# Kernel tuning notes

Hardware: AMD Instinct MI355X
Metric: run time of the kernel (lower is better)

The kernel has to match this reference:

```python
import jax, jax.numpy as jnp
import numpy as np
from jax import lax

RATE = 2
KSIZE = 3
FUSE_K = 3
SOFTMAX_SCALE = 10.0
EPS = 1e-8


def extract_patches(x, k, s):
    """ZeroPad2d(1) then unfold: x [B,C,H,W] -> patches [B, oh*ow, C, k, k]."""
    xp = jnp.pad(x, ((0, 0), (0, 0), (1, 1), (1, 1)))
    B, C, Hp, Wp = xp.shape
    oh = (Hp - k) // s + 1
    ow = (Wp - k) // s + 1
    ii = (jnp.arange(oh) * s)[:, None] + jnp.arange(k)[None, :]   # [oh,k]
    jj = (jnp.arange(ow) * s)[:, None] + jnp.arange(k)[None, :]   # [ow,k]
    p = xp[:, :, ii[:, :, None, None], jj[None, None, :, :]]      # [B,C,oh,k,ow,k]
    p = p.transpose(0, 2, 4, 1, 3, 5).reshape(B, oh * ow, C, k, k)
    return p


def _fuse_conv(a, eye):
    # a: [B,1,N,M]; 3x3 identity-diagonal smoothing conv, padding 1
    return lax.conv_general_dilated(a, eye, (1, 1), [(1, 1), (1, 1)],
                                    dimension_numbers=('NCHW', 'OIHW', 'NCHW'))


def contextual_attention(in_data, mask):
    B, C, H, W = in_data.shape
    Cf = C // 2
    f_full = in_data[:, :Cf]          # narrow(1,0,C//2)
    b_full = in_data[:, :Cf]          # source narrows the SAME slice for b
    mask_f = mask.astype(in_data.dtype)
    rate = RATE
    kernel = 2 * rate

    # raw 4x4 patches of full-res background (deconv filters), [B,L,Cf,4,4]
    raw_w = extract_patches(b_full, kernel, rate)

    # nearest downsample by 1/rate == strided slicing
    f = f_full[:, :, ::rate, ::rate]
    b = b_full[:, :, ::rate, ::rate]
    h, w = f.shape[2], f.shape[3]
    L = h * w

    # 3x3 matching patches of downsampled background, L2-normalized per patch
    wpat = extract_patches(b, KSIZE, 1)                              # [B,L,Cf,3,3]
    norm = jnp.sqrt(jnp.sum(wpat * wpat, axis=(2, 3, 4), keepdims=True))
    wn = wpat / jnp.maximum(norm, EPS)

    # per-sample conv2d(xi, wi_normed, padding=1) == patch/patch correlation
    fp = extract_patches(f, KSIZE, 1)                                # [B,hw,Cf,3,3]
    yi = jnp.einsum('bpckl,bqckl->bqp', fp, wn).reshape(B, L, h, w)  # [B,L,h,w]

    # fuse: two diagonal 3x3 smoothing passes over the [L, h*w] score matrix
    eye = jnp.eye(FUSE_K, dtype=in_data.dtype).reshape(1, 1, FUSE_K, FUSE_K)
    A = yi.reshape(B, 1, L, h * w)
    A = _fuse_conv(A, eye)
    A = A.reshape(B, h, w, h, w).transpose(0, 2, 1, 4, 3).reshape(B, 1, w * h, w * h)
    A = _fuse_conv(A, eye)
    A = A.reshape(B, w, h, w, h).transpose(0, 2, 1, 4, 3)
    yi = A.reshape(B, L, h, w)

    # mask gate: mm = 1 where the 3x3 mask patch is all-zero
    mpat = extract_patches(mask_f, KSIZE, 1)[0]                      # [L,1,3,3]
    m_mean = jnp.mean(mpat, axis=(1, 2, 3))                          # [L]
    mm = (m_mean == 0.0).astype(in_data.dtype)[None, :, None, None]
    yi = yi * mm
    yi = jax.nn.softmax(yi * SOFTMAX_SCALE, axis=1)
    yi = yi * mm

    # conv_transpose2d(yi, raw_wi, stride=rate, padding=1) / 4 per sample
    def agg(y1, rw):
        rhs = jnp.flip(rw, (-2, -1)).transpose(1, 0, 2, 3)           # [Cf,L,4,4]
        return lax.conv_general_dilated(y1[None], rhs, (1, 1), [(2, 2), (2, 2)],
                                        lhs_dilation=(rate, rate),
                                        dimension_numbers=('NCHW', 'OIHW', 'NCHW'))[0]
    y = jax.vmap(agg)(yi, raw_w) / 4.0                               # [B,Cf,H,W]

    # masked_fill_(inv_mask, 0) == multiply by {0,1} mask, upsampled to H x W
    mask_up = jnp.repeat(jnp.repeat(mask_f, rate, axis=2), rate, axis=3)
    y = y * mask_up

    return jnp.concatenate([b_full, f_full, y], axis=1)             # [B,3*Cf,H,W]


def setup_inputs() -> dict:
    key = jax.random.key(0)
    k1, k2 = jax.random.split(key)
    in_data = jax.random.normal(k1, (2, 128, 128, 128), dtype=jnp.float32)
    mask = jax.random.randint(k2, (1, 1, 64, 64), 0, 2, dtype=jnp.int32)
    return {"in_data": in_data, "mask": mask}


def reference(in_data, mask):
    return contextual_attention(in_data, mask)
```

## Files before the change

kernel.cpp:

```cpp
#include <hip/hip_runtime.h>
#include <math.h>

#define MAX_SLOTS 64
#define L 4096

#define OFF_CNT   0
#define OFF_LIST  64
#define OFF_FSUB  512
#define OFF_K5    2230784
#define OFF_SF    4065792

__global__ __launch_bounds__(256) void k_init(const float* __restrict__ in,
                                              const int* __restrict__ mask,
                                              int* __restrict__ cnt,
                                              int* __restrict__ list,
                                              float* __restrict__ fsub,
                                              float* __restrict__ sf) {
    int idx = blockIdx.x * 256 + threadIdx.x;
    int j = idx & 63;
    int i = (idx >> 6) & 63;
    int c = (idx >> 12) & 63;
    int b = idx >> 18;
    float v = in[(((b * 128 + c) * 128) + 2 * i) * 128 + 2 * j];
    fsub[(size_t)b * 278784 + c * 4356 + (i + 1) * 66 + (j + 1)] = v;
    sf[idx] = 0.f;
    if (idx < 33280) {
        int plane = idx / 260;
        int r = idx - plane * 260;
        int pb = plane >> 6, pc = plane & 63;
        int row, col;
        if (r < 66) { row = 0; col = r; }
        else if (r < 132) { row = 65; col = r - 66; }
        else { int rr = r - 132; row = (rr >> 1) + 1; col = (rr & 1) ? 65 : 0; }
        fsub[(size_t)pb * 278784 + pc * 4356 + row * 66 + col] = 0.f;
    }
    if (blockIdx.x == 0) {
        __shared__ int lcnt;
        if (threadIdx.x == 0) lcnt = 0;
        __syncthreads();
        for (int q = threadIdx.x; q < L; q += 256) {
            int qi = q >> 6, qj = q & 63;
            bool allz = true;
            for (int dy = -1; dy <= 1; ++dy)
                for (int dx = -1; dx <= 1; ++dx) {
                    int y = qi + dy, x = qj + dx;
                    if (y >= 0 && y < 64 && x >= 0 && x < 64)
                        allz = allz && (mask[y * 64 + x] == 0);
                }
            if (allz) {
                int p = atomicAdd(&lcnt, 1);
                if (p < MAX_SLOTS) list[p] = q;
            }
        }
        __syncthreads();
        if (threadIdx.x == 0) *cnt = (lcnt < MAX_SLOTS) ? lcnt : MAX_SLOTS;
    }
}

__global__ __launch_bounds__(256) void k_mid(const int* __restrict__ cnt,
                                             const int* __restrict__ list,
                                             const float* __restrict__ fsub,
                                             float* __restrict__ K5,
                                             float* __restrict__ sf) {
    __shared__ float smem[5184];
    __shared__ int iflags[16];
    int tid = threadIdx.x;
    int blk = blockIdx.x;
    int nact = min(*cnt, MAX_SLOTS);

    if (blk < 128) {
        int slot = blk & 63, b = blk >> 6;
        if (slot >= nact) {
            for (int t = tid; t < 1600; t += 256) {
                int c = t / 25, e = t - c * 25;
                K5[(((size_t)b * 64 + c) * 64 + slot) * 28 + e] = 0.f;
            }
            return;
        }
        float* patch9 = smem;
        if (tid < 9) iflags[tid] = 0;
        __syncthreads();
        int Q = list[slot];
        const float* F = fsub + (size_t)b * 278784;
        int w = tid >> 6, lane = tid & 63;
        for (int combo = w; combo < 9; combo += 4) {
            int d2 = combo / 3 - 1, d1 = combo % 3 - 1;
            int XQ = ((Q & 63) << 6) + (Q >> 6) + d2;
            if (XQ < 0 || XQ >= L) continue;
            int YQ = ((XQ & 63) << 6) + (XQ >> 6);
            int R = YQ + d1;
            if (R < 0 || R >= L) continue;
            if (lane == 0) iflags[combo] = 1;
            int ri = R >> 6, rj = R & 63;
            const float* Fp = F + ri * 66 + rj;
            float vals[9]; float ss = 0.f;
            #pragma unroll
            for (int k = 0; k < 9; ++k) {
                int t = lane + (k << 6);
                int c = t / 9; int tap = t - c * 9;
                int dy = tap / 3, dx = tap - dy * 3;
                float v = Fp[c * 4356 + dy * 66 + dx];
                vals[k] = v; ss += v * v;
            }
            for (int o = 32; o > 0; o >>= 1) ss += __shfl_xor(ss, o);
            float inv = 1.f / fmaxf(sqrtf(ss), 1e-8f);
            float* dst = patch9 + combo * 576;
            #pragma unroll
            for (int k = 0; k < 9; ++k) dst[lane + (k << 6)] = vals[k] * inv;
        }
        __syncthreads();
        for (int t = tid; t < 1600; t += 256) {
            int c = t / 25, e = t - c * 25;
            int oy = e / 5 - 2, ox = e - (e / 5) * 5 - 2;
            float s = 0.f;
            for (int dy = -1; dy <= 1; ++dy) {
                int dd2 = oy - dy; if (dd2 < -1 || dd2 > 1) continue;
                for (int dx = -1; dx <= 1; ++dx) {
                    int dd1 = ox - dx; if (dd1 < -1 || dd1 > 1) continue;
                    int combo = (dd2 + 1) * 3 + (dd1 + 1);
                    if (iflags[combo])
                        s += patch9[combo * 576 + c * 9 + (dy + 1) * 3 + (dx + 1)];
                }
            }
            K5[(((size_t)b * 64 + c) * 64 + slot) * 28 + e] = s;
        }
        return;
    }

    int bt = blk - 128;
    int combo = bt % 9; int rest = bt / 9;
    int slot = rest & 63, b = rest >> 6;
    if (slot >= nact) return;
    int d2 = combo / 3 - 1, d1 = combo % 3 - 1;
    int Q = list[slot];
    int XQ = ((Q & 63) << 6) + (Q >> 6) + d2;
    if (XQ < 0 || XQ >= L) return;
    int YQ = ((XQ & 63) << 6) + (XQ >> 6);
    int R = YQ + d1;
    if (R < 0 || R >= L) return;
    int ri = R >> 6, rj = R & 63;
    const float* F = fsub + (size_t)b * 278784;
    float* patch = smem;
    float* red = smem + 576;
    const float* Fp = F + ri * 66 + rj;
    auto ld = [&](int t) -> float {
        int c = t / 9; int tap = t - c * 9;
        int dy = tap / 3, dx = tap - dy * 3;
        return Fp[c * 4356 + dy * 66 + dx];
    };
    float v0 = ld(tid), v1 = ld(tid + 256), v2 = (tid < 64) ? ld(tid + 512) : 0.f;
    red[tid] = v0 * v0 + v1 * v1 + v2 * v2;
    __syncthreads();
    if (tid < 64) {
        float a = red[tid] + red[tid + 64] + red[tid + 128] + red[tid + 192];
        for (int o = 32; o > 0; o >>= 1) a += __shfl_xor(a, o);
        if (tid == 0) smem[832] = 1.f / fmaxf(sqrtf(a), 1e-8f);
    }
    __syncthreads();
    float inv = smem[832];
    patch[tid] = v0 * inv; patch[tid + 256] = v1 * inv;
    if (tid < 64) patch[tid + 512] = v2 * inv;
    __syncthreads();
    if (tid >= 252) return;
    int i, j;
    if (tid < 64)       { i = 0;  j = tid; }
    else if (tid < 128) { i = 63; j = tid - 64; }
    else if (tid < 190) { i = tid - 127; j = 0; }
    else                { i = tid - 189; j = 63; }
    int P = (i << 6) + j;
    int XP = (j << 6) + i + d2;
    if (XP < 0 || XP >= L) return;
    int YP = ((XP & 63) << 6) + (XP >> 6);
    int Z = YP + d1;
    if (Z < 0 || Z >= L) return;
    int pi = Z >> 6, pj = Z & 63;
    const float* Fz = F + pi * 66 + pj;
    float dot = 0.f;
    #pragma unroll 4
    for (int c = 0; c < 64; ++c) {
        const float* Fc = Fz + c * 4356;
        const float* pc = patch + c * 9;
        dot += Fc[0] * pc[0]   + Fc[1] * pc[1]   + Fc[2] * pc[2];
        dot += Fc[66] * pc[3]  + Fc[67] * pc[4]  + Fc[68] * pc[5];
        dot += Fc[132] * pc[6] + Fc[133] * pc[7] + Fc[134] * pc[8];
    }
    atomicAdd(&sf[((size_t)b * 64 + slot) * 4096 + P], dot);
}

__global__ __launch_bounds__(256) void k_conv(const float* __restrict__ fsub,
                                              const int* __restrict__ cnt,
                                              const float* __restrict__ K5,
                                              float* __restrict__ sf) {
    int nact = min(*cnt, MAX_SLOTS);
    if (nact == 0) return;
    int wid = __builtin_amdgcn_readfirstlane(blockIdx.x * 4 + (threadIdx.x >> 6));
    int j = threadIdx.x & 63;
    int r   = 1 + (wid % 62);
    int cg2 = (wid / 62) & 15;
    int b   = wid / 992;
    int jc = min(max(j, 1), 62);
    const float* F = fsub + (size_t)b * 278784;
    int base = (r - 1) * 66 + (jc - 1);
    bool active = (j >= 1 && j <= 62);
    int P = (r << 6) + j;
    for (int s0 = 0; s0 < nact; s0 += 16) {
        float acc[16];
        #pragma unroll
        for (int s = 0; s < 16; ++s) acc[s] = 0.f;
        #pragma unroll
        for (int cc = 0; cc < 4; ++cc) {
            int c = cg2 * 4 + cc;
            const float* Fc = F + c * 4356 + base;
            float win[25];
            #pragma unroll
            for (int dy = 0; dy < 5; ++dy)
                #pragma unroll
                for (int dx = 0; dx < 5; ++dx)
                    win[dy * 5 + dx] = Fc[dy * 66 + dx];
            const float* kc = K5 + (((size_t)b * 64 + c) * 64 + s0) * 28;
            #pragma unroll
            for (int s = 0; s < 16; ++s) {
                #pragma unroll
                for (int k = 0; k < 25; ++k)
                    acc[s] += kc[s * 28 + k] * win[k];
            }
        }
        if (active) {
            int smax = min(16, nact - s0);
            for (int s = 0; s < smax; ++s)
                atomicAdd(&sf[((size_t)b * 64 + (s0 + s)) * 4096 + P], acc[s]);
        }
    }
}

__global__ __launch_bounds__(256) void k_tail(const float* __restrict__ in,
                                              const int* __restrict__ mask,
                                              const int* __restrict__ cnt,
                                              const int* __restrict__ list,
                                              const float* __restrict__ sf,
                                              float* __restrict__ out) {
    __shared__ float sw[MAX_SLOTS * 192];
    __shared__ float pat8[MAX_SLOTS * 128];
    int tid = threadIdx.x;
    int nact = min(*cnt, MAX_SLOTS);
    int up = blockIdx.x, cg8 = blockIdx.y, b = blockIdx.z;
    int c0 = cg8 * 8;
    const float* inb0 = in + (size_t)b * 2097152 + (size_t)c0 * 16384;
    const float* sfb = sf + (size_t)b * 64 * 4096;
    for (int t = tid; t < nact * 192; t += 256) {
        int s = t / 192; int rr = t - s * 192;
        int i = up - 1 + (rr >> 6); int jj = rr & 63;
        sw[t] = (i >= 0 && i < 64) ? sfb[(size_t)s * 4096 + (i << 6) + jj] : 0.f;
    }
    for (int t = tid; t < nact * 128; t += 256) {
        int s = t >> 7; int rr = t & 127;
        int cc = rr >> 4; int e = rr & 15; int aa = e >> 2; int bb = e & 3;
        int q = list[s]; int qi = q >> 6, qj = q & 63;
        int row = 2 * qi - 1 + aa, col = 2 * qj - 1 + bb;
        float v = (row >= 0 && row < 128 && col >= 0 && col < 128)
                  ? inb0[(size_t)cc * 16384 + row * 128 + col] : 0.f;
        pat8[t] = v;
    }
    __syncthreads();
    if (tid < 192 && nact > 0) {
        int i = up - 1 + (tid >> 6);
        if (i >= 0 && i < 64) {
            float M = 0.f;
            for (int s = 0; s < nact; ++s)
                M = fmaxf(M, 10.f * sw[s * 192 + tid]);
            float den = (float)(L - nact) * expf(-M);
            for (int s = 0; s < nact; ++s) {
                float e = expf(10.f * sw[s * 192 + tid] - M);
                sw[s * 192 + tid] = e;
                den += e;
            }
            float inv = 1.f / den;
            for (int s = 0; s < nact; ++s)
                sw[s * 192 + tid] *= inv;
        } else {
            for (int s = 0; s < nact; ++s) sw[s * 192 + tid] = 0.f;
        }
    }
    __syncthreads();
    int uu = tid >> 7, v = tid & 127;
    int u = up * 2 + uu;
    float y[8];
    #pragma unroll
    for (int cc = 0; cc < 8; ++cc) y[cc] = 0.f;
    if (mask[(u >> 1) * 64 + (v >> 1)] != 0 && nact > 0) {
        int pa = (u + 1) & 1, pb = (v + 1) & 1;
        int i0 = (u + 1 - pa) >> 1, j0 = (v + 1 - pb) >> 1;
        int Wp[4]; int tap[4]; bool val[4];
        #pragma unroll
        for (int di = 0; di < 2; ++di)
            #pragma unroll
            for (int dj = 0; dj < 2; ++dj) {
                int p = di * 2 + dj;
                int i = i0 - di, j = j0 - dj;
                int ii = i - (up - 1);
                val[p] = (j >= 0 && j < 64);
                Wp[p] = val[p] ? (ii * 64 + j) : 0;
                tap[p] = (pa + 2 * di) * 4 + (pb + 2 * dj);
            }
        for (int s = 0; s < nact; ++s) {
            const float* wrow = sw + s * 192;
            const float* ps = pat8 + s * 128;
            #pragma unroll
            for (int p = 0; p < 4; ++p) {
                if (!val[p]) continue;
                float wv = wrow[Wp[p]];
                #pragma unroll
                for (int cc = 0; cc < 8; ++cc)
                    y[cc] += wv * ps[cc * 16 + tap[p]];
            }
        }
        #pragma unroll
        for (int cc = 0; cc < 8; ++cc) y[cc] *= 0.25f;
    }
    size_t ob = (size_t)(b * 192) * 16384 + (size_t)u * 128 + v;
    #pragma unroll
    for (int cc = 0; cc < 8; ++cc) {
        int c = c0 + cc;
        float pval = in[(size_t)(b * 128 + c) * 16384 + u * 128 + v];
        out[ob + (size_t)c * 16384] = pval;
        out[ob + (size_t)(c + 64) * 16384] = pval;
        out[ob + (size_t)(c + 128) * 16384] = y[cc];
    }
}

extern "C" void kernel_launch(void* const* d_in, const int* in_sizes, int n_in,
                              void* d_out, int out_size, void* d_ws, size_t ws_size,
                              hipStream_t stream) {
    const float* in = (const float*)d_in[0];
    const int* mask = (const int*)d_in[1];
    float* out = (float*)d_out;
    char* ws = (char*)d_ws;
    int* cnt    = (int*)(ws + OFF_CNT);
    int* list   = (int*)(ws + OFF_LIST);
    float* fsub = (float*)(ws + OFF_FSUB);
    float* K5   = (float*)(ws + OFF_K5);
    float* sf   = (float*)(ws + OFF_SF);

    k_init<<<2048, 256, 0, stream>>>(in, mask, cnt, list, fsub, sf);
    k_mid<<<1280, 256, 0, stream>>>(cnt, list, fsub, K5, sf);
    k_conv<<<496, 256, 0, stream>>>(fsub, cnt, K5, sf);
    k_tail<<<dim3(64, 8, 2), 256, 0, stream>>>(in, mask, cnt, list, sf, out);
}
```

Baseline: 148.5 us.

## Merge pipeline into three kernels and stream softmax weights in tiles

Every block that builds K5 now computes the mask list redundantly in shared memory, using a parallel bitmask and prefix scan. The K5 construction reads directly from the input, so it can run in the same launch as the fsub init. The conv and the correlation-score kernels are merged into one launch, removing one kernel boundary. The pass-through output copies move into the front kernel, and the tail kernel computes softmax stats once, then processes slots in tiles of 16 with smaller shared memory. This raises occupancy at the cost of recomputing exp and repeating the mask scan.

```diff
diff --git a/kernel.cpp b/kernel.cpp
--- a/kernel.cpp
+++ b/kernel.cpp
@@ -10,13 +10,128 @@
 #define OFF_K5    2230784
 #define OFF_SF    4065792
 
-__global__ __launch_bounds__(256) void k_init(const float* __restrict__ in,
-                                              const int* __restrict__ mask,
-                                              int* __restrict__ cnt,
-                                              int* __restrict__ list,
-                                              float* __restrict__ fsub,
-                                              float* __restrict__ sf) {
-    int idx = blockIdx.x * 256 + threadIdx.x;
+__device__ __forceinline__ void build_list(const int* __restrict__ mask,
+                                           unsigned int* flagw, int* llist,
+                                           int* lcnt) {
+    int tid = threadIdx.x;
+    for (int w = tid; w < 128; w += 256) flagw[w] = 0u;
+    __syncthreads();
+    int q0 = tid * 16;
+    unsigned int mybits = 0u;
+    for (int k = 0; k < 16; ++k) {
+        int q = q0 + k;
+        int qi = q >> 6, qj = q & 63;
+        bool allz = true;
+        for (int dy = -1; dy <= 1; ++dy)
+            for (int dx = -1; dx <= 1; ++dx) {
+                int y = qi + dy, x = qj + dx;
+                if (y >= 0 && y < 64 && x >= 0 && x < 64)
+                    allz = allz && (mask[y * 64 + x] == 0);
+            }
+        if (allz) mybits |= (1u << k);
+    }
+    if (mybits) atomicOr(&flagw[q0 >> 5], mybits << (q0 & 31));
+    __syncthreads();
+    if (tid < 64) {
+        unsigned int w0 = flagw[2 * tid], w1 = flagw[2 * tid + 1];
+        int own = __popc(w0) + __popc(w1);
+        int inc = own;
+        for (int o = 1; o < 64; o <<= 1) {
+            int v = __shfl_up(inc, o);
+            if (tid >= o) inc += v;
+        }
+        int pos = inc - own;
+        for (int k = 0; k < 32; ++k)
+            if (w0 & (1u << k)) { if (pos < MAX_SLOTS) llist[pos] = tid * 64 + k; ++pos; }
+        for (int k = 0; k < 32; ++k)
+            if (w1 & (1u << k)) { if (pos < MAX_SLOTS) llist[pos] = tid * 64 + 32 + k; ++pos; }
+        if (tid == 63) *lcnt = (inc < MAX_SLOTS) ? inc : MAX_SLOTS;
+    }
+    __syncthreads();
+}
+
+__global__ __launch_bounds__(256) void k_front(const float* __restrict__ in,
+                                               const int* __restrict__ mask,
+                                               int* __restrict__ cnt,
+                                               int* __restrict__ list,
+                                               float* __restrict__ fsub,
+                                               float* __restrict__ K5,
+                                               float* __restrict__ sf,
+                                               float* __restrict__ out) {
+    __shared__ float patch9[5184];
+    __shared__ unsigned int flagw[128];
+    __shared__ int llist[MAX_SLOTS];
+    __shared__ int lcnt;
+    __shared__ int iflags[16];
+    int tid = threadIdx.x;
+    int blk = blockIdx.x;
+
+    if (blk < 128) {
+        int slot = blk & 63, b = blk >> 6;
+        build_list(mask, flagw, llist, &lcnt);
+        int nact = lcnt;
+        if (blk == 0) {
+            if (tid < MAX_SLOTS) list[tid] = llist[tid];
+            if (tid == 64) *cnt = nact;
+        }
+        if (slot >= nact) {
+            for (int t = tid; t < 1600; t += 256) {
+                int c = t / 25, e = t - c * 25;
+                K5[(((size_t)b * 64 + c) * 64 + slot) * 28 + e] = 0.f;
+            }
+            return;
+        }
+        if (tid < 16) iflags[tid] = 0;
+        __syncthreads();
+        int Q = llist[slot];
+        const float* inb = in + (size_t)b * 2097152;
+        int w = tid >> 6, lane = tid & 63;
+        for (int combo = w; combo < 9; combo += 4) {
+            int d2 = combo / 3 - 1, d1 = combo % 3 - 1;
+            int XQ = ((Q & 63) << 6) + (Q >> 6) + d2;
+            if (XQ < 0 || XQ >= L) continue;
+            int YQ = ((XQ & 63) << 6) + (XQ >> 6);
+            int R = YQ + d1;
+            if (R < 0 || R >= L) continue;
+            if (lane == 0) iflags[combo] = 1;
+            int ri = R >> 6, rj = R & 63;
+            float vals[9]; float ss = 0.f;
+            #pragma unroll
+            for (int k = 0; k < 9; ++k) {
+                int t = lane + (k << 6);
+                int c = t / 9; int tap = t - c * 9;
+                int dy = tap / 3, dx = tap - dy * 3;
+                int yy = ri + dy - 1, xx = rj + dx - 1;
+                float v = ((unsigned)yy < 64u && (unsigned)xx < 64u)
+                          ? inb[((size_t)c << 14) + (yy << 8) + (xx << 1)] : 0.f;
+                vals[k] = v; ss += v * v;
+            }
+            for (int o = 32; o > 0; o >>= 1) ss += __shfl_xor(ss, o);
+            float inv = 1.f / fmaxf(sqrtf(ss), 1e-8f);
+            float* dst = patch9 + combo * 576;
+            #pragma unroll
+            for (int k = 0; k < 9; ++k) dst[lane + (k << 6)] = vals[k] * inv;
+        }
+        __syncthreads();
+        for (int t = tid; t < 1600; t += 256) {
+            int c = t / 25, e = t - c * 25;
+            int oy = e / 5 - 2, ox = e - (e / 5) * 5 - 2;
+            float s = 0.f;
+            for (int dy = -1; dy <= 1; ++dy) {
+                int dd2 = oy - dy; if (dd2 < -1 || dd2 > 1) continue;
+                for (int dx = -1; dx <= 1; ++dx) {
+                    int dd1 = ox - dx; if (dd1 < -1 || dd1 > 1) continue;
+                    int combo = (dd2 + 1) * 3 + (dd1 + 1);
+                    if (iflags[combo])
+                        s += patch9[combo * 576 + c * 9 + (dy + 1) * 3 + (dx + 1)];
+                }
+            }
+            K5[(((size_t)b * 64 + c) * 64 + slot) * 28 + e] = s;
+        }
+        return;
+    }
+
+    int idx = (blk - 128) * 256 + tid;
     int j = idx & 63;
     int i = (idx >> 6) & 63;
     int c = (idx >> 12) & 63;
@@ -34,100 +149,73 @@
         else { int rr = r - 132; row = (rr >> 1) + 1; col = (rr & 1) ? 65 : 0; }
         fsub[(size_t)pb * 278784 + pc * 4356 + row * 66 + col] = 0.f;
     }
-    if (blockIdx.x == 0) {
-        __shared__ int lcnt;
-        if (threadIdx.x == 0) lcnt = 0;
-        __syncthreads();
-        for (int q = threadIdx.x; q < L; q += 256) {
-            int qi = q >> 6, qj = q & 63;
-            bool allz = true;
-            for (int dy = -1; dy <= 1; ++dy)
-                for (int dx = -1; dx <= 1; ++dx) {
-                    int y = qi + dy, x = qj + dx;
-                    if (y >= 0 && y < 64 && x >= 0 && x < 64)
-                        allz = allz && (mask[y * 64 + x] == 0);
-                }
-            if (allz) {
-                int p = atomicAdd(&lcnt, 1);
-                if (p < MAX_SLOTS) list[p] = q;
-            }
-        }
-        __syncthreads();
-        if (threadIdx.x == 0) *cnt = (lcnt < MAX_SLOTS) ? lcnt : MAX_SLOTS;
-    }
-}
-
-__global__ __launch_bounds__(256) void k_mid(const int* __restrict__ cnt,
-                                             const int* __restrict__ list,
-                                             const float* __restrict__ fsub,
-                                             float* __restrict__ K5,
-                                             float* __restrict__ sf) {
-    __shared__ float smem[5184];
-    __shared__ int iflags[16];
+    #pragma unroll
+    for (int k = 0; k < 4; ++k) {
+        int t = idx + k * 524288;
+        int pix = t & 16383;
+        int cc = (t >> 14) & 63;
+        int bb = t >> 20;
+        float pv = in[(size_t)(bb * 128 + cc) * 16384 + pix];
+        size_t ob = (size_t)bb * 3145728;
+        out[ob + (size_t)cc * 16384 + pix] = pv;
+        out[ob + (size_t)(cc + 64) * 16384 + pix] = pv;
+    }
+}
+
+__global__ __launch_bounds__(256) void k_mid2(const int* __restrict__ cnt,
+                                              const int* __restrict__ list,
+                                              const float* __restrict__ fsub,
+                                              const float* __restrict__ K5,
+                                              float* __restrict__ sf) {
+    __shared__ float smem[840];
     int tid = threadIdx.x;
     int blk = blockIdx.x;
     int nact = min(*cnt, MAX_SLOTS);
-
-    if (blk < 128) {
-        int slot = blk & 63, b = blk >> 6;
-        if (slot >= nact) {
-            for (int t = tid; t < 1600; t += 256) {
-                int c = t / 25, e = t - c * 25;
-                K5[(((size_t)b * 64 + c) * 64 + slot) * 28 + e] = 0.f;
-            }
-            return;
-        }
-        float* patch9 = smem;
-        if (tid < 9) iflags[tid] = 0;
-        __syncthreads();
-        int Q = list[slot];
+    if (nact == 0) return;
+
+    if (blk < 496) {
+        int wid = __builtin_amdgcn_readfirstlane(blk * 4 + (tid >> 6));
+        int j = tid & 63;
+        int r   = 1 + (wid % 62);
+        int cg2 = (wid / 62) & 15;
+        int b   = wid / 992;
+        int jc = min(max(j, 1), 62);
         const float* F = fsub + (size_t)b * 278784;
-        int w = tid >> 6, lane = tid & 63;
-        for (int combo = w; combo < 9; combo += 4) {
-            int d2 = combo / 3 - 1, d1 = combo % 3 - 1;
-            int XQ = ((Q & 63) << 6) + (Q >> 6) + d2;
-            if (XQ < 0 || XQ >= L) continue;
-            int YQ = ((XQ & 63) << 6) + (XQ >> 6);
-            int R = YQ + d1;
-            if (R < 0 || R >= L) continue;
-            if (lane == 0) iflags[combo] = 1;
-            int ri = R >> 6, rj = R & 63;
-            const float* Fp = F + ri * 66 + rj;
-            float vals[9]; float ss = 0.f;
-            #pragma unroll
-            for (int k = 0; k < 9; ++k) {
-                int t = lane + (k << 6);
-                int c = t / 9; int tap = t - c * 9;
-                int dy = tap / 3, dx = tap - dy * 3;
-                float v = Fp[c * 4356 + dy * 66 + dx];
-                vals[k] = v; ss += v * v;
-            }
-            for (int o = 32; o > 0; o >>= 1) ss += __shfl_xor(ss, o);
-            float inv = 1.f / fmaxf(sqrtf(ss), 1e-8f);
-            float* dst = patch9 + combo * 576;
-            #pragma unroll
-            for (int k = 0; k < 9; ++k) dst[lane + (k << 6)] = vals[k] * inv;
-        }
-        __syncthreads();
-        for (int t = tid; t < 1600; t += 256) {
-            int c = t / 25, e = t - c * 25;
-            int oy = e / 5 - 2, ox = e - (e / 5) * 5 - 2;
-            float s = 0.f;
-            for (int dy = -1; dy <= 1; ++dy) {
-                int dd2 = oy - dy; if (dd2 < -1 || dd2 > 1) continue;
-                for (int dx = -1; dx <= 1; ++dx) {
-                    int dd1 = ox - dx; if (dd1 < -1 || dd1 > 1) continue;
-                    int combo = (dd2 + 1) * 3 + (dd1 + 1);
-                    if (iflags[combo])
-                        s += patch9[combo * 576 + c * 9 + (dy + 1) * 3 + (dx + 1)];
+        int base = (r - 1) * 66 + (jc - 1);
+        bool active = (j >= 1 && j <= 62);
+        int P = (r << 6) + j;
+        for (int s0 = 0; s0 < nact; s0 += 16) {
+            float acc[16];
+            #pragma unroll
+            for (int s = 0; s < 16; ++s) acc[s] = 0.f;
+            #pragma unroll
+            for (int cc = 0; cc < 4; ++cc) {
+                int c = cg2 * 4 + cc;
+                const float* Fc = F + c * 4356 + base;
+                float win[25];
+                #pragma unroll
+                for (int dy = 0; dy < 5; ++dy)
+                    #pragma unroll
+                    for (int dx = 0; dx < 5; ++dx)
+                        win[dy * 5 + dx] = Fc[dy * 66 + dx];
+                const float* kc = K5 + (((size_t)b * 64 + c) * 64 + s0) * 28;
+                #pragma unroll
+                for (int s = 0; s < 16; ++s) {
+                    #pragma unroll
+                    for (int k = 0; k < 25; ++k)
+                        acc[s] += kc[s * 28 + k] * win[k];
                 }
             }
-            K5[(((size_t)b * 64 + c) * 64 + slot) * 28 + e] = s;
+            if (active) {
+                int smax = min(16, nact - s0);
+                for (int s = 0; s < smax; ++s)
+                    atomicAdd(&sf[((size_t)b * 64 + (s0 + s)) * 4096 + P], acc[s]);
+            }
         }
         return;
     }
 
-    int bt = blk - 128;
+    int bt = blk - 496;
     int combo = bt % 9; int rest = bt / 9;
     int slot = rest & 63, b = rest >> 6;
     if (slot >= nact) return;
@@ -187,145 +275,105 @@
     atomicAdd(&sf[((size_t)b * 64 + slot) * 4096 + P], dot);
 }
 
-__global__ __launch_bounds__(256) void k_conv(const float* __restrict__ fsub,
-                                              const int* __restrict__ cnt,
-                                              const float* __restrict__ K5,
-                                              float* __restrict__ sf) {
-    int nact = min(*cnt, MAX_SLOTS);
-    if (nact == 0) return;
-    int wid = __builtin_amdgcn_readfirstlane(blockIdx.x * 4 + (threadIdx.x >> 6));
-    int j = threadIdx.x & 63;
-    int r   = 1 + (wid % 62);
-    int cg2 = (wid / 62) & 15;
-    int b   = wid / 992;
-    int jc = min(max(j, 1), 62);
-    const float* F = fsub + (size_t)b * 278784;
-    int base = (r - 1) * 66 + (jc - 1);
-    bool active = (j >= 1 && j <= 62);
-    int P = (r << 6) + j;
-    for (int s0 = 0; s0 < nact; s0 += 16) {
-        float acc[16];
-        #pragma unroll
-        for (int s = 0; s < 16; ++s) acc[s] = 0.f;
-        #pragma unroll
-        for (int cc = 0; cc < 4; ++cc) {
-            int c = cg2 * 4 + cc;
-            const float* Fc = F + c * 4356 + base;
-            float win[25];
-            #pragma unroll
-            for (int dy = 0; dy < 5; ++dy)
-                #pragma unroll
-                for (int dx = 0; dx < 5; ++dx)
-                    win[dy * 5 + dx] = Fc[dy * 66 + dx];
-            const float* kc = K5 + (((size_t)b * 64 + c) * 64 + s0) * 28;
-            #pragma unroll
-            for (int s = 0; s < 16; ++s) {
-                #pragma unroll
-                for (int k = 0; k < 25; ++k)
-                    acc[s] += kc[s * 28 + k] * win[k];
-            }
-        }
-        if (active) {
-            int smax = min(16, nact - s0);
-            for (int s = 0; s < smax; ++s)
-                atomicAdd(&sf[((size_t)b * 64 + (s0 + s)) * 4096 + P], acc[s]);
-        }
-    }
-}
-
-__global__ __launch_bounds__(256) void k_tail(const float* __restrict__ in,
-                                              const int* __restrict__ mask,
-                                              const int* __restrict__ cnt,
-                                              const int* __restrict__ list,
-                                              const float* __restrict__ sf,
-                                              float* __restrict__ out) {
-    __shared__ float sw[MAX_SLOTS * 192];
-    __shared__ float pat8[MAX_SLOTS * 128];
+__global__ __launch_bounds__(256) void k_tail2(const float* __restrict__ in,
+                                               const int* __restrict__ mask,
+                                               const int* __restrict__ cnt,
+                                               const int* __restrict__ list,
+                                               const float* __restrict__ sf,
+                                               float* __restrict__ out) {
+    __shared__ float sw16[16 * 192];
+    __shared__ float pat16[16 * 128];
+    __shared__ float Mv[192];
+    __shared__ float Dv[192];
     int tid = threadIdx.x;
     int nact = min(*cnt, MAX_SLOTS);
     int up = blockIdx.x, cg8 = blockIdx.y, b = blockIdx.z;
     int c0 = cg8 * 8;
     const float* inb0 = in + (size_t)b * 2097152 + (size_t)c0 * 16384;
-    const float* sfb = sf + (size_t)b * 64 * 4096;
-    for (int t = tid; t < nact * 192; t += 256) {
-        int s = t / 192; int rr = t - s * 192;
-        int i = up - 1 + (rr >> 6); int jj = rr & 63;
-        sw[t] = (i >= 0 && i < 64) ? sfb[(size_t)s * 4096 + (i << 6) + jj] : 0.f;
-    }
-    for (int t = tid; t < nact * 128; t += 256) {
-        int s = t >> 7; int rr = t & 127;
-        int cc = rr >> 4; int e = rr & 15; int aa = e >> 2; int bb = e & 3;
-        int q = list[s]; int qi = q >> 6, qj = q & 63;
-        int row = 2 * qi - 1 + aa, col = 2 * qj - 1 + bb;
-        float v = (row >= 0 && row < 128 && col >= 0 && col < 128)
-                  ? inb0[(size_t)cc * 16384 + row * 128 + col] : 0.f;
-        pat8[t] = v;
-    }
-    __syncthreads();
-    if (tid < 192 && nact > 0) {
-        int i = up - 1 + (tid >> 6);
-        if (i >= 0 && i < 64) {
-            float M = 0.f;
+    const float* sfb = sf + (size_t)b * 262144;
+
+    if (tid < 192) {
+        int i = up - 1 + (tid >> 6); int jj = tid & 63;
+        float M = 0.f, invden = 0.f;
+        if ((unsigned)i < 64u && nact > 0) {
+            const float* sp = sfb + (i << 6) + jj;
             for (int s = 0; s < nact; ++s)
-                M = fmaxf(M, 10.f * sw[s * 192 + tid]);
+                M = fmaxf(M, 10.f * sp[(size_t)s * 4096]);
             float den = (float)(L - nact) * expf(-M);
-            for (int s = 0; s < nact; ++s) {
-                float e = expf(10.f * sw[s * 192 + tid] - M);
-                sw[s * 192 + tid] = e;
-                den += e;
-            }
-            float inv = 1.f / den;
             for (int s = 0; s < nact; ++s)
-                sw[s * 192 + tid] *= inv;
-        } else {
-            for (int s = 0; s < nact; ++s) sw[s * 192 + tid] = 0.f;
-        }
-    }
-    __syncthreads();
+                den += expf(10.f * sp[(size_t)s * 4096] - M);
+            invden = 1.f / den;
+        }
+        Mv[tid] = M; Dv[tid] = invden;
+    }
+
     int uu = tid >> 7, v = tid & 127;
     int u = up * 2 + uu;
+    bool gate = (mask[(u >> 1) * 64 + (v >> 1)] != 0) && (nact > 0);
+    int Wp[4]; int tap[4]; bool val[4];
+    {
+        int pa = (u + 1) & 1, pb_ = (v + 1) & 1;
+        int i0 = (u + 1 - pa) >> 1, j0 = (v + 1 - pb_) >> 1;
+        #pragma unroll
+        for (int di = 0; di < 2; ++di)
+            #pragma unroll
+            for (int dj = 0; dj < 2; ++dj) {
+                int p = di * 2 + dj;
+                int ii = i0 - di, jx = j0 - dj;
+                int iis = ii - (up - 1);
+                val[p] = (jx >= 0 && jx < 64);
+                Wp[p] = val[p] ? (iis * 64 + jx) : 0;
+                tap[p] = (pa + 2 * di) * 4 + (pb_ + 2 * dj);
+            }
+    }
     float y[8];
     #pragma unroll
     for (int cc = 0; cc < 8; ++cc) y[cc] = 0.f;
-    if (mask[(u >> 1) * 64 + (v >> 1)] != 0 && nact > 0) {
-        int pa = (u + 1) & 1, pb = (v + 1) & 1;
-        int i0 = (u + 1 - pa) >> 1, j0 = (v + 1 - pb) >> 1;
-        int Wp[4]; int tap[4]; bool val[4];
-        #pragma unroll
-        for (int di = 0; di < 2; ++di)
-            #pragma unroll
-            for (int dj = 0; dj < 2; ++dj) {
-                int p = di * 2 + dj;
-                int i = i0 - di, j = j0 - dj;
-                int ii = i - (up - 1);
-                val[p] = (j >= 0 && j < 64);
-                Wp[p] = val[p] ? (ii * 64 + j) : 0;
-                tap[p] = (pa + 2 * di) * 4 + (pb + 2 * dj);
-            }
-        for (int s = 0; s < nact; ++s) {
-            const float* wrow = sw + s * 192;
-            const float* ps = pat8 + s * 128;
-            #pragma unroll
-            for (int p = 0; p < 4; ++p) {
-                if (!val[p]) continue;
-                float wv = wrow[Wp[p]];
+
+    for (int s0 = 0; s0 < nact; s0 += 16) {
+        int ns = min(16, nact - s0);
+        __syncthreads();
+        for (int t = tid; t < ns * 192; t += 256) {
+            int sl = t / 192; int rr = t - sl * 192;
+            int i = up - 1 + (rr >> 6); int jj = rr & 63;
+            float wv = 0.f;
+            if ((unsigned)i < 64u)
+                wv = expf(10.f * sfb[(size_t)(s0 + sl) * 4096 + (i << 6) + jj] - Mv[rr]) * Dv[rr];
+            sw16[t] = wv;
+        }
+        for (int t = tid; t < ns * 128; t += 256) {
+            int sl = t >> 7; int rr = t & 127;
+            int cc = rr >> 4; int e = rr & 15; int aa = e >> 2; int bb = e & 3;
+            int q = list[s0 + sl]; int qi = q >> 6, qj = q & 63;
+            int row = 2 * qi - 1 + aa, col = 2 * qj - 1 + bb;
+            float pv = (row >= 0 && row < 128 && col >= 0 && col < 128)
+                       ? inb0[(size_t)cc * 16384 + row * 128 + col] : 0.f;
+            pat16[t] = pv;
+        }
+        __syncthreads();
+        if (gate) {
+            for (int s = 0; s < ns; ++s) {
+                const float* wrow = sw16 + s * 192;
+                const float* ps = pat16 + s * 128;
                 #pragma unroll
-                for (int cc = 0; cc < 8; ++cc)
-                    y[cc] += wv * ps[cc * 16 + tap[p]];
-            }
-        }
+                for (int p = 0; p < 4; ++p) {
+                    if (!val[p]) continue;
+                    float wv = wrow[Wp[p]];
+                    #pragma unroll
+                    for (int cc = 0; cc < 8; ++cc)
+                        y[cc] += wv * ps[cc * 16 + tap[p]];
+                }
+            }
+        }
+    }
+    if (gate) {
         #pragma unroll
         for (int cc = 0; cc < 8; ++cc) y[cc] *= 0.25f;
     }
-    size_t ob = (size_t)(b * 192) * 16384 + (size_t)u * 128 + v;
+    size_t ob = (size_t)b * 3145728 + (size_t)(c0 + 128) * 16384 + (size_t)u * 128 + v;
     #pragma unroll
-    for (int cc = 0; cc < 8; ++cc) {
-        int c = c0 + cc;
-        float pval = in[(size_t)(b * 128 + c) * 16384 + u * 128 + v];
-        out[ob + (size_t)c * 16384] = pval;
-        out[ob + (size_t)(c + 64) * 16384] = pval;
-        out[ob + (size_t)(c + 128) * 16384] = y[cc];
-    }
+    for (int cc = 0; cc < 8; ++cc)
+        out[ob + (size_t)cc * 16384] = y[cc];
 }
 
 extern "C" void kernel_launch(void* const* d_in, const int* in_sizes, int n_in,
@@ -341,8 +389,7 @@
     float* K5   = (float*)(ws + OFF_K5);
     float* sf   = (float*)(ws + OFF_SF);
 
-    k_init<<<2048, 256, 0, stream>>>(in, mask, cnt, list, fsub, sf);
-    k_mid<<<1280, 256, 0, stream>>>(cnt, list, fsub, K5, sf);
-    k_conv<<<496, 256, 0, stream>>>(fsub, cnt, K5, sf);
-    k_tail<<<dim3(64, 8, 2), 256, 0, stream>>>(in, mask, cnt, list, sf, out);
-}
+    k_front<<<2176, 256, 0, stream>>>(in, mask, cnt, list, fsub, K5, sf, out);
+    k_mid2<<<1648, 256, 0, stream>>>(cnt, list, fsub, K5, sf);
+    k_tail2<<<dim3(64, 8, 2), 256, 0, stream>>>(in, mask, cnt, list, sf, out);
+}
```

New measurement: 146.0 us. Within noise of the previous version (-1.7%).
